# Performance work log

Measured on AMD Instinct MI355X. Metric: run time of the kernel, lower is better.

## Reference

```python
import jax, jax.numpy as jnp
import numpy as np

VOCAB = 100000
EMB = 100
HID = 100
CTX_LEN = 60          # must equal MAX_DESC_LEN for linear_1 to fit
FACT_LEN = 20
DESC_LEN = 60


def setup_inputs() -> dict:
    key = jax.random.key(0)
    ks = jax.random.split(key, 12)
    s = 0.05
    context = jax.random.randint(ks[0], (CTX_LEN, FACT_LEN), 1, VOCAB)
    fact_lengths = jax.random.randint(ks[1], (CTX_LEN,), 1, FACT_LEN)
    description = jax.random.randint(ks[2], (DESC_LEN,), 1, VOCAB)
    emb_ctx = jax.random.normal(ks[3], (VOCAB, EMB), jnp.float32) * s
    emb_ctx = emb_ctx.at[0].set(0.0)  # padding_idx=0
    emb_dec = jax.random.normal(ks[4], (VOCAB, EMB), jnp.float32) * s
    emb_dec = emb_dec.at[0].set(0.0)
    w1 = jax.random.normal(ks[5], (HID, CTX_LEN * HID), jnp.float32) * s
    b1 = jax.random.normal(ks[6], (HID,), jnp.float32) * s
    w_ih = jax.random.normal(ks[7], (3 * HID, EMB), jnp.float32) * s
    w_hh = jax.random.normal(ks[8], (3 * HID, HID), jnp.float32) * s
    b_ih = jax.random.normal(ks[9], (3 * HID,), jnp.float32) * s
    b_hh = jax.random.normal(ks[10], (3 * HID,), jnp.float32) * s
    w_out = jax.random.normal(ks[11], (VOCAB, HID), jnp.float32) * s
    b_out = jnp.zeros((VOCAB,), jnp.float32)
    return {"context": context, "fact_lengths": fact_lengths, "description": description,
            "emb_ctx": emb_ctx, "emb_dec": emb_dec, "w1": w1, "b1": b1,
            "w_ih": w_ih, "w_hh": w_hh, "b_ih": b_ih, "b_hh": b_hh,
            "w_out": w_out, "b_out": b_out}


def _forward(context, description, emb_ctx, emb_dec, w1, b1,
             w_ih, w_hh, b_ih, b_hh, w_out, b_out):
    # ---- InputModule: embed + positional fact encoder ----
    emb = emb_ctx[context]                       # [CTX_LEN, FACT_LEN, EMB]
    slen, elen = FACT_LEN, EMB
    s = jnp.arange(slen, dtype=jnp.float32) / (slen - 1)   # [slen]
    e = jnp.arange(elen, dtype=jnp.float32) / (elen - 1)   # [elen]
    l = 1.0 - s[:, None] - e[None, :] * (1.0 - 2.0 * s[:, None])  # [slen, elen]
    facts = jnp.sum(emb * l[None], axis=1)       # [CTX_LEN, EMB]

    # ---- initial decoder hidden from flattened facts ----
    h0 = facts.reshape(1, -1) @ w1.T + b1        # [1, HID]

    x0 = emb_dec[1][None, :]                     # SOS token embedding [1, EMB]

    def step(carry, tok):
        h, x = carry
        gi = x @ w_ih.T + b_ih                   # [1, 3H]
        gh = h @ w_hh.T + b_hh
        i_r, i_z, i_n = jnp.split(gi, 3, axis=-1)
        h_r, h_z, h_n = jnp.split(gh, 3, axis=-1)
        r = jax.nn.sigmoid(i_r + h_r)
        z = jax.nn.sigmoid(i_z + h_z)
        n = jnp.tanh(i_n + r * h_n)
        h_new = (1.0 - z) * n + z * h            # [1, HID]
        logits = h_new @ w_out.T + b_out         # [1, VOCAB]
        logp = jax.nn.log_softmax(logits, axis=-1)
        loss_t = -logp[0, tok]                   # NLLLoss, batch 1
        x_next = emb_dec[tok][None, :]           # teacher forcing
        return (h_new, x_next), loss_t

    (_, _), losses = jax.lax.scan(step, (h0, x0), description)
    return jnp.sum(losses).reshape(1)            # matches torch FloatTensor([.])


def reference(context, fact_lengths, description, emb_ctx, emb_dec, w1, b1,
              w_ih, w_hh, b_ih, b_hh, w_out, b_out):
    # fact_lengths is unused by the original forward (PositionalFactEncoder ignores it)
    return _forward(context, description, emb_ctx, emb_dec, w1, b1,
                    w_ih, w_hh, b_ih, b_hh, w_out, b_out)
```

## Files before the change

### kernel.cpp

```cpp
#include <hip/hip_runtime.h>
#include <hip/hip_bf16.h>
#include <math.h>

#define VOCAB 100000
#define EMB 100
#define HID 100
#define CTX_LEN 60
#define FACT_LEN 20
#define DESC_LEN 60
#define NCHUNK (VOCAB / 16)
#define NWAVES 1024

#define WS_FACTS 0
#define WS_X     6000
#define WS_H0    12000
#define WS_GI    12160
#define WS_H     30160
#define WS_MS    36864

typedef __attribute__((ext_vector_type(8))) short short8;
typedef __attribute__((ext_vector_type(4))) float f32x4;

static __device__ __forceinline__ unsigned short f2bf(float f) {
    union { float f; unsigned u; } x; x.f = f;
    unsigned r = (x.u + 0x7FFFu + ((x.u >> 16) & 1u)) >> 16;
    return (unsigned short)r;
}

__global__ __launch_bounds__(128) void k1_prep(const int* __restrict__ context,
                                               const int* __restrict__ desc,
                                               const float* __restrict__ emb_ctx,
                                               const float* __restrict__ emb_dec,
                                               float* __restrict__ ws,
                                               float* __restrict__ out) {
    int b = blockIdx.x, tid = threadIdx.x;
    if (b < 60) {
        __shared__ int toks[20];
        if (tid < 20) toks[tid] = context[b * 20 + tid];
        __syncthreads();
        if (tid < 100) {
            float ef = tid * (1.f / 99.f);
            float acc = 0.f;
            #pragma unroll
            for (int s = 0; s < 20; s++) {
                float sf = s * (1.f / 19.f);
                float l = 1.f - sf - ef * (1.f - 2.f * sf);
                acc = fmaf(emb_ctx[toks[s] * 100 + tid], l, acc);
            }
            ws[WS_FACTS + b * 100 + tid] = acc;
        }
    } else {
        int t = b - 60;
        int tok = (t == 0) ? 1 : desc[t - 1];
        if (tid < 100) ws[WS_X + t * 100 + tid] = emb_dec[tok * 100 + tid];
        if (b == 60 && tid == 0) out[0] = 0.f;
    }
}

__global__ __launch_bounds__(320) void k2_h0_gi(const float* __restrict__ w1,
                                                const float* __restrict__ b1,
                                                const float* __restrict__ w_ih,
                                                const float* __restrict__ b_ih,
                                                float* __restrict__ ws) {
    int b = blockIdx.x, tid = threadIdx.x;
    if (b < 100) {
        __shared__ float red[320];
        const float* facts = ws + WS_FACTS;
        const float* wr = w1 + b * 6000;
        float p = 0.f;
        for (int k = tid; k < 6000; k += 320) p = fmaf(facts[k], wr[k], p);
        red[tid] = p; __syncthreads();
        if (tid < 64) red[tid] += red[256 + tid];
        __syncthreads();
        for (int st = 128; st > 0; st >>= 1) {
            if (tid < st) red[tid] += red[tid + st];
            __syncthreads();
        }
        if (tid == 0) ws[WS_H0 + b] = red[0] + b1[b];
    } else {
        int t = b - 100;
        __shared__ float xs[100];
        if (tid < 100) xs[tid] = ws[WS_X + t * 100 + tid];
        __syncthreads();
        if (tid < 300) {
            float p = b_ih[tid];
            const float* wr = w_ih + tid * 100;
            #pragma unroll 4
            for (int k = 0; k < 100; k++) p = fmaf(wr[k], xs[k], p);
            ws[WS_GI + t * 300 + tid] = p;
        }
    }
}

__global__ __launch_bounds__(320, 1) void k3_gru(const float* __restrict__ w_hh,
                                                 const float* __restrict__ b_hh,
                                                 float* __restrict__ ws) {
    __shared__ float gi_lds[18000];
    __shared__ float gh_lds[320];
    __shared__ __align__(16) unsigned short h_bf[128];

    const int tid = threadIdx.x;
    const int wave = tid >> 6, lane = tid & 63;
    const int q = lane >> 4, n = lane & 15;

    short8 bfr[16];
    #pragma unroll
    for (int i = 0; i < 4; i++) {
        int row = (wave * 4 + i) * 16 + n;
        const float* wr = w_hh + row * 100;
        #pragma unroll
        for (int kt = 0; kt < 4; kt++) {
            int k0 = kt * 32 + q * 8;
            float va[8];
            #pragma unroll
            for (int jj = 0; jj < 8; jj++) va[jj] = 0.f;
            if (row < 300) {
                if (k0 + 4 <= 100) {
                    float4 a = *(const float4*)(wr + k0);
                    va[0] = a.x; va[1] = a.y; va[2] = a.z; va[3] = a.w;
                }
                if (k0 + 8 <= 100) {
                    float4 b = *(const float4*)(wr + k0 + 4);
                    va[4] = b.x; va[5] = b.y; va[6] = b.z; va[7] = b.w;
                }
            }
            short8 f;
            #pragma unroll
            for (int jj = 0; jj < 8; jj++) f[jj] = (short)f2bf(va[jj]);
            bfr[i * 4 + kt] = f;
        }
    }

    for (int k = tid; k < 18000; k += 320) gi_lds[k] = ws[WS_GI + k];

    float hreg = 0.f, bh0 = 0.f, bh1 = 0.f, bh2 = 0.f;
    if (tid < 100) {
        hreg = ws[WS_H0 + tid];
        h_bf[tid] = f2bf(hreg);
        bh0 = b_hh[tid]; bh1 = b_hh[100 + tid]; bh2 = b_hh[200 + tid];
    } else if (tid < 128) {
        h_bf[tid] = 0;
    }
    __syncthreads();

    float* H = ws + WS_H;
    for (int t = 0; t < 60; t++) {
        short8 afr[4];
        #pragma unroll
        for (int kt = 0; kt < 4; kt++)
            afr[kt] = *(const short8*)&h_bf[kt * 32 + q * 8];
        #pragma unroll
        for (int i = 0; i < 4; i++) {
            f32x4 a = {0.f, 0.f, 0.f, 0.f};
            a = __builtin_amdgcn_mfma_f32_16x16x32_bf16(afr[0], bfr[i * 4 + 0], a, 0, 0, 0);
            a = __builtin_amdgcn_mfma_f32_16x16x32_bf16(afr[1], bfr[i * 4 + 1], a, 0, 0, 0);
            a = __builtin_amdgcn_mfma_f32_16x16x32_bf16(afr[2], bfr[i * 4 + 2], a, 0, 0, 0);
            a = __builtin_amdgcn_mfma_f32_16x16x32_bf16(afr[3], bfr[i * 4 + 3], a, 0, 0, 0);
            if (lane < 16) gh_lds[(wave * 4 + i) * 16 + lane] = a[0];
        }
        __syncthreads();
        if (tid < 100) {
            float gir = gi_lds[t * 300 + tid];
            float giz = gi_lds[t * 300 + 100 + tid];
            float gin = gi_lds[t * 300 + 200 + tid];
            float ghr = gh_lds[tid] + bh0;
            float ghz = gh_lds[100 + tid] + bh1;
            float ghn = gh_lds[200 + tid] + bh2;
            float r = 1.f / (1.f + __expf(-(gir + ghr)));
            float z = 1.f / (1.f + __expf(-(giz + ghz)));
            float a = fmaf(r, ghn, gin);
            float tt = __expf(-2.f * fabsf(a));
            float nn = copysignf((1.f - tt) / (1.f + tt), a);
            hreg = (1.f - z) * nn + z * hreg;
            h_bf[tid] = f2bf(hreg);
            H[t * 100 + tid] = hreg;
        }
        __syncthreads();
    }
}

__global__ __launch_bounds__(256, 1) void k4_logits(const float* __restrict__ w_out,
                                                    const float* __restrict__ b_out,
                                                    float* __restrict__ ws) {
    const float* H = ws + WS_H;
    float* ms = ws + WS_MS;
    const int lane = threadIdx.x & 63;
    const int gw = blockIdx.x * 4 + (threadIdx.x >> 6);
    const int q = lane >> 4, n = lane & 15;
    const int k_base = q * 8;

    short8 afr[4][4];
    #pragma unroll
    for (int mt = 0; mt < 4; mt++) {
        int m = mt * 16 + n;
        #pragma unroll
        for (int kt = 0; kt < 4; kt++) {
            int k0 = kt * 32 + k_base;
            float va[8];
            #pragma unroll
            for (int jj = 0; jj < 8; jj++) va[jj] = 0.f;
            if (m < 60) {
                if (k0 + 4 <= 100) {
                    float4 a = *(const float4*)(H + m * 100 + k0);
                    va[0] = a.x; va[1] = a.y; va[2] = a.z; va[3] = a.w;
                }
                if (k0 + 8 <= 100) {
                    float4 b = *(const float4*)(H + m * 100 + k0 + 4);
                    va[4] = b.x; va[5] = b.y; va[6] = b.z; va[7] = b.w;
                }
            }
            short8 f;
            #pragma unroll
            for (int jj = 0; jj < 8; jj++) f[jj] = (short)f2bf(va[jj]);
            afr[mt][kt] = f;
        }
    }

    float mS[16], sS[16];
    #pragma unroll
    for (int i = 0; i < 16; i++) { mS[i] = -3.0e38f; sS[i] = 0.f; }

    for (int c = gw; c < NCHUNK; c += NWAVES) {
        int row = c * 16 + n;
        short8 bfr[4];
        #pragma unroll
        for (int kt = 0; kt < 4; kt++) {
            int k0 = kt * 32 + k_base;
            float va[8];
            #pragma unroll
            for (int jj = 0; jj < 8; jj++) va[jj] = 0.f;
            if (k0 + 4 <= 100) {
                float4 a = *(const float4*)(w_out + row * 100 + k0);
                va[0] = a.x; va[1] = a.y; va[2] = a.z; va[3] = a.w;
            }
            if (k0 + 8 <= 100) {
                float4 b = *(const float4*)(w_out + row * 100 + k0 + 4);
                va[4] = b.x; va[5] = b.y; va[6] = b.z; va[7] = b.w;
            }
            short8 f;
            #pragma unroll
            for (int jj = 0; jj < 8; jj++) f[jj] = (short)f2bf(va[jj]);
            bfr[kt] = f;
        }
        float bo = b_out[row];
        #pragma unroll
        for (int mt = 0; mt < 4; mt++) {
            f32x4 acc = {0.f, 0.f, 0.f, 0.f};
            acc = __builtin_amdgcn_mfma_f32_16x16x32_bf16(afr[mt][0], bfr[0], acc, 0, 0, 0);
            acc = __builtin_amdgcn_mfma_f32_16x16x32_bf16(afr[mt][1], bfr[1], acc, 0, 0, 0);
            acc = __builtin_amdgcn_mfma_f32_16x16x32_bf16(afr[mt][2], bfr[2], acc, 0, 0, 0);
            acc = __builtin_amdgcn_mfma_f32_16x16x32_bf16(afr[mt][3], bfr[3], acc, 0, 0, 0);
            #pragma unroll
            for (int reg = 0; reg < 4; reg++) {
                float x = acc[reg] + bo;
                int i = mt * 4 + reg;
                float mo = mS[i];
                float mn = fmaxf(mo, x);
                sS[i] = sS[i] * __expf(mo - mn) + __expf(x - mn);
                mS[i] = mn;
            }
        }
    }

    #pragma unroll
    for (int i = 0; i < 16; i++) {
        float m = mS[i], s = sS[i];
        #pragma unroll
        for (int off = 1; off < 16; off <<= 1) {
            float m2 = __shfl_xor(m, off);
            float s2 = __shfl_xor(s, off);
            float mn = fmaxf(m, m2);
            s = s * __expf(m - mn) + s2 * __expf(m2 - mn);
            m = mn;
        }
        mS[i] = m; sS[i] = s;
    }
    if (n == 0) {
        #pragma unroll
        for (int mt = 0; mt < 4; mt++) {
            #pragma unroll
            for (int reg = 0; reg < 4; reg++) {
                int t = mt * 16 + q * 4 + reg;
                int i = mt * 4 + reg;
                if (t < 60) {
                    float2 val; val.x = mS[i]; val.y = sS[i];
                    ((float2*)ms)[t * NWAVES + gw] = val;
                }
            }
        }
    }
}

__global__ __launch_bounds__(256) void k5_final(const int* __restrict__ desc,
                                                const float* __restrict__ w_out,
                                                const float* __restrict__ b_out,
                                                const float* __restrict__ ws,
                                                float* __restrict__ out) {
    int t = blockIdx.x, tid = threadIdx.x;
    __shared__ float sm[256], ss[256], sd[256];
    const float2* ms = (const float2*)(ws + WS_MS);
    float m = -3.0e38f, s = 0.f;
    for (int i = tid; i < NWAVES; i += 256) {
        float2 p = ms[t * NWAVES + i];
        float mn = fmaxf(m, p.x);
        s = s * __expf(m - mn) + p.y * __expf(p.x - mn);
        m = mn;
    }
    sm[tid] = m; ss[tid] = s; __syncthreads();
    for (int st = 128; st > 0; st >>= 1) {
        if (tid < st) {
            float mo = sm[tid], so = ss[tid];
            float m2 = sm[tid + st], s2 = ss[tid + st];
            float mn = fmaxf(mo, m2);
            sm[tid] = mn;
            ss[tid] = so * __expf(mo - mn) + s2 * __expf(m2 - mn);
        }
        __syncthreads();
    }
    int tok = desc[t];
    float p = 0.f;
    if (tid < 100) p = ws[WS_H + t * 100 + tid] * w_out[tok * 100 + tid];
    sd[tid] = p; __syncthreads();
    for (int st = 128; st > 0; st >>= 1) {
        if (tid < st) sd[tid] += sd[tid + st];
        __syncthreads();
    }
    if (tid == 0) {
        float logit = sd[0] + b_out[tok];
        float loss = sm[0] + logf(ss[0]) - logit;
        atomicAdd(out, loss);
    }
}

extern "C" void kernel_launch(void* const* d_in, const int* in_sizes, int n_in,
                              void* d_out, int out_size, void* d_ws, size_t ws_size,
                              hipStream_t stream) {
    const int*   context = (const int*)d_in[0];
    const int*   desc    = (const int*)d_in[2];
    const float* emb_ctx = (const float*)d_in[3];
    const float* emb_dec = (const float*)d_in[4];
    const float* w1      = (const float*)d_in[5];
    const float* b1      = (const float*)d_in[6];
    const float* w_ih    = (const float*)d_in[7];
    const float* w_hh    = (const float*)d_in[8];
    const float* b_ih    = (const float*)d_in[9];
    const float* b_hh    = (const float*)d_in[10];
    const float* w_out   = (const float*)d_in[11];
    const float* b_out   = (const float*)d_in[12];
    float* out = (float*)d_out;
    float* ws  = (float*)d_ws;

    k1_prep  <<<120, 128, 0, stream>>>(context, desc, emb_ctx, emb_dec, ws, out);
    k2_h0_gi <<<160, 320, 0, stream>>>(w1, b1, w_ih, b_ih, ws);
    k3_gru   <<<1,   320, 0, stream>>>(w_hh, b_hh, ws);
    k4_logits<<<256, 256, 0, stream>>>(w_out, b_out, ws);
    k5_final <<<60,  256, 0, stream>>>(desc, w_out, b_out, ws, out);
}
```

Measured before the change: 204.0 us.

## Make GRU gates wave-local via shuffles and widen logits grid

The GRU kernel now arranges the w_hh rows so each wave owns 20 hidden units across all three gates. The gate sums are gathered with lane shuffles instead of a shared-memory round trip, which removes one block barrier per timestep. The MFMA chains are split into two independent accumulators, and the hidden history is kept in LDS and written out once at the end. The logits kernel grid grows from 256 to 1024 blocks, with a fallback to 256 if the workspace is too small. This adds more partial max/sum pairs for the final reduction kernel to combine.

After: 214.4 us. +5.0%, slower.

```diff
diff --git a/kernel.cpp b/kernel.cpp
--- a/kernel.cpp
+++ b/kernel.cpp
@@ -9,7 +9,6 @@
 #define FACT_LEN 20
 #define DESC_LEN 60
 #define NCHUNK (VOCAB / 16)
-#define NWAVES 1024
 
 #define WS_FACTS 0
 #define WS_X     6000
@@ -95,26 +94,37 @@
 __global__ __launch_bounds__(320, 1) void k3_gru(const float* __restrict__ w_hh,
                                                  const float* __restrict__ b_hh,
                                                  float* __restrict__ ws) {
-    __shared__ float gi_lds[18000];
-    __shared__ float gh_lds[320];
+    __shared__ __align__(16) float gi_lds[18000];
+    __shared__ __align__(16) float h_hist[6000];
     __shared__ __align__(16) unsigned short h_bf[128];
 
     const int tid = threadIdx.x;
     const int wave = tid >> 6, lane = tid & 63;
     const int q = lane >> 4, n = lane & 15;
+    const int l = lane;
+    const int j = 20 * wave + l;
 
     short8 bfr[16];
     #pragma unroll
     for (int i = 0; i < 4; i++) {
-        int row = (wave * 4 + i) * 16 + n;
-        const float* wr = w_hh + row * 100;
+        int row;
+        if (i == 0)      row = 20 * wave + n;
+        else if (i == 1) row = 100 + 20 * wave + n;
+        else if (i == 2) row = 200 + 20 * wave + n;
+        else {
+            if (n < 4)       row = 20 * wave + 16 + n;
+            else if (n < 8)  row = 100 + 20 * wave + 12 + n;
+            else if (n < 12) row = 200 + 20 * wave + 8 + n;
+            else             row = -1;
+        }
+        const float* wr = w_hh + (row < 0 ? 0 : row) * 100;
         #pragma unroll
         for (int kt = 0; kt < 4; kt++) {
             int k0 = kt * 32 + q * 8;
             float va[8];
             #pragma unroll
             for (int jj = 0; jj < 8; jj++) va[jj] = 0.f;
-            if (row < 300) {
+            if (row >= 0) {
                 if (k0 + 4 <= 100) {
                     float4 a = *(const float4*)(wr + k0);
                     va[0] = a.x; va[1] = a.y; va[2] = a.z; va[3] = a.w;
@@ -131,57 +141,80 @@
         }
     }
 
-    for (int k = tid; k < 18000; k += 320) gi_lds[k] = ws[WS_GI + k];
+    {
+        const float4* g4 = (const float4*)(ws + WS_GI);
+        float4* l4 = (float4*)gi_lds;
+        for (int k = tid; k < 4500; k += 320) l4[k] = g4[k];
+    }
 
     float hreg = 0.f, bh0 = 0.f, bh1 = 0.f, bh2 = 0.f;
-    if (tid < 100) {
-        hreg = ws[WS_H0 + tid];
-        h_bf[tid] = f2bf(hreg);
-        bh0 = b_hh[tid]; bh1 = b_hh[100 + tid]; bh2 = b_hh[200 + tid];
-    } else if (tid < 128) {
-        h_bf[tid] = 0;
-    }
+    if (l < 20) {
+        hreg = ws[WS_H0 + j];
+        bh0 = b_hh[j]; bh1 = b_hh[100 + j]; bh2 = b_hh[200 + j];
+        h_bf[j] = f2bf(hreg);
+    }
+    if (tid >= 100 && tid < 128) h_bf[tid] = 0;
     __syncthreads();
 
-    float* H = ws + WS_H;
+    const int s_lo  = (l < 16) ? l : 0;
+    const int s3r   = (l < 16) ? 0 : (l - 16);
+    const int s3z   = (l < 16) ? 4 : (l - 12);
+    const int s3n   = (l < 16) ? 8 : (l - 8);
+
     for (int t = 0; t < 60; t++) {
         short8 afr[4];
         #pragma unroll
         for (int kt = 0; kt < 4; kt++)
             afr[kt] = *(const short8*)&h_bf[kt * 32 + q * 8];
+
+        float val[4];
         #pragma unroll
         for (int i = 0; i < 4; i++) {
-            f32x4 a = {0.f, 0.f, 0.f, 0.f};
-            a = __builtin_amdgcn_mfma_f32_16x16x32_bf16(afr[0], bfr[i * 4 + 0], a, 0, 0, 0);
-            a = __builtin_amdgcn_mfma_f32_16x16x32_bf16(afr[1], bfr[i * 4 + 1], a, 0, 0, 0);
-            a = __builtin_amdgcn_mfma_f32_16x16x32_bf16(afr[2], bfr[i * 4 + 2], a, 0, 0, 0);
-            a = __builtin_amdgcn_mfma_f32_16x16x32_bf16(afr[3], bfr[i * 4 + 3], a, 0, 0, 0);
-            if (lane < 16) gh_lds[(wave * 4 + i) * 16 + lane] = a[0];
-        }
-        __syncthreads();
-        if (tid < 100) {
-            float gir = gi_lds[t * 300 + tid];
-            float giz = gi_lds[t * 300 + 100 + tid];
-            float gin = gi_lds[t * 300 + 200 + tid];
-            float ghr = gh_lds[tid] + bh0;
-            float ghz = gh_lds[100 + tid] + bh1;
-            float ghn = gh_lds[200 + tid] + bh2;
+            f32x4 z4 = {0.f, 0.f, 0.f, 0.f};
+            f32x4 a01 = __builtin_amdgcn_mfma_f32_16x16x32_bf16(afr[0], bfr[i * 4 + 0], z4, 0, 0, 0);
+            a01 = __builtin_amdgcn_mfma_f32_16x16x32_bf16(afr[1], bfr[i * 4 + 1], a01, 0, 0, 0);
+            f32x4 a23 = __builtin_amdgcn_mfma_f32_16x16x32_bf16(afr[2], bfr[i * 4 + 2], z4, 0, 0, 0);
+            a23 = __builtin_amdgcn_mfma_f32_16x16x32_bf16(afr[3], bfr[i * 4 + 3], a23, 0, 0, 0);
+            val[i] = a01[0] + a23[0];
+        }
+
+        float v0  = __shfl(val[0], s_lo, 64);
+        float v1  = __shfl(val[1], s_lo, 64);
+        float v2  = __shfl(val[2], s_lo, 64);
+        float w3r = __shfl(val[3], s3r, 64);
+        float w3z = __shfl(val[3], s3z, 64);
+        float w3n = __shfl(val[3], s3n, 64);
+
+        if (l < 20) {
+            float ghr = ((l < 16) ? v0 : w3r) + bh0;
+            float ghz = ((l < 16) ? v1 : w3z) + bh1;
+            float ghn = ((l < 16) ? v2 : w3n) + bh2;
+            float gir = gi_lds[t * 300 + j];
+            float giz = gi_lds[t * 300 + 100 + j];
+            float gin = gi_lds[t * 300 + 200 + j];
             float r = 1.f / (1.f + __expf(-(gir + ghr)));
             float z = 1.f / (1.f + __expf(-(giz + ghz)));
             float a = fmaf(r, ghn, gin);
             float tt = __expf(-2.f * fabsf(a));
             float nn = copysignf((1.f - tt) / (1.f + tt), a);
             hreg = (1.f - z) * nn + z * hreg;
-            h_bf[tid] = f2bf(hreg);
-            H[t * 100 + tid] = hreg;
-        }
-        __syncthreads();
+            h_bf[j] = f2bf(hreg);
+            h_hist[t * 100 + j] = hreg;
+        }
+        __syncthreads();
+    }
+
+    {
+        float4* Hg = (float4*)(ws + WS_H);
+        const float4* h4 = (const float4*)h_hist;
+        for (int k = tid; k < 1500; k += 320) Hg[k] = h4[k];
     }
 }
 
 __global__ __launch_bounds__(256, 1) void k4_logits(const float* __restrict__ w_out,
                                                     const float* __restrict__ b_out,
-                                                    float* __restrict__ ws) {
+                                                    float* __restrict__ ws,
+                                                    int nwaves) {
     const float* H = ws + WS_H;
     float* ms = ws + WS_MS;
     const int lane = threadIdx.x & 63;
@@ -220,7 +253,7 @@
     #pragma unroll
     for (int i = 0; i < 16; i++) { mS[i] = -3.0e38f; sS[i] = 0.f; }
 
-    for (int c = gw; c < NCHUNK; c += NWAVES) {
+    for (int c = gw; c < NCHUNK; c += nwaves) {
         int row = c * 16 + n;
         short8 bfr[4];
         #pragma unroll
@@ -284,7 +317,7 @@
                 int i = mt * 4 + reg;
                 if (t < 60) {
                     float2 val; val.x = mS[i]; val.y = sS[i];
-                    ((float2*)ms)[t * NWAVES + gw] = val;
+                    ((float2*)ms)[t * nwaves + gw] = val;
                 }
             }
         }
@@ -295,13 +328,14 @@
                                                 const float* __restrict__ w_out,
                                                 const float* __restrict__ b_out,
                                                 const float* __restrict__ ws,
-                                                float* __restrict__ out) {
+                                                float* __restrict__ out,
+                                                int nwaves) {
     int t = blockIdx.x, tid = threadIdx.x;
     __shared__ float sm[256], ss[256], sd[256];
     const float2* ms = (const float2*)(ws + WS_MS);
     float m = -3.0e38f, s = 0.f;
-    for (int i = tid; i < NWAVES; i += 256) {
-        float2 p = ms[t * NWAVES + i];
+    for (int i = tid; i < nwaves; i += 256) {
+        float2 p = ms[t * nwaves + i];
         float mn = fmaxf(m, p.x);
         s = s * __expf(m - mn) + p.y * __expf(p.x - mn);
         m = mn;
@@ -350,9 +384,14 @@
     float* out = (float*)d_out;
     float* ws  = (float*)d_ws;
 
+    int nblocks = 1024;
+    size_t need = (size_t)(WS_MS + 60 * (nblocks * 4) * 2) * 4;
+    if (ws_size < need) nblocks = 256;
+    int nwaves = nblocks * 4;
+
     k1_prep  <<<120, 128, 0, stream>>>(context, desc, emb_ctx, emb_dec, ws, out);
     k2_h0_gi <<<160, 320, 0, stream>>>(w1, b1, w_ih, b_ih, ws);
     k3_gru   <<<1,   320, 0, stream>>>(w_hh, b_hh, ws);
-    k4_logits<<<256, 256, 0, stream>>>(w_out, b_out, ws);
-    k5_final <<<60,  256, 0, stream>>>(desc, w_out, b_out, ws, out);
-}
+    k4_logits<<<nblocks, 256, 0, stream>>>(w_out, b_out, ws, nwaves);
+    k5_final <<<60,  256, 0, stream>>>(desc, w_out, b_out, ws, out, nwaves);
+}
```
